# Performance work log

Hardware: AMD Instinct MI355X
Metric: run time of the kernel (lower is better)

## Reference

```python
import math
import jax, jax.numpy as jnp
import numpy as np

NUM_HEADS = 4
HEAD_DIM = 384


def reshape_fortran(x, shape):
    # column-major (Fortran) reshape, matching the torch reverse-permute trick
    x = jnp.transpose(x, tuple(reversed(range(x.ndim))))
    x = x.reshape(tuple(reversed(shape)))
    return jnp.transpose(x, tuple(reversed(range(len(shape)))))


def rel_pos_rotate(data):
    # data: [b, n_heads, L=2M-1, S] -> [b, n_heads, S, S]
    data = jnp.transpose(data, (0, 2, 3, 1))  # [b, d0=L, d1=S, d2=H]
    b, d0, d1, d2 = data.shape
    data = jnp.concatenate([data, jnp.zeros((b, d1, d1, d2), data.dtype)], axis=1)
    data = reshape_fortran(data, (b, (d0 + d1) * d1, 1, d2))
    data = data[:, :(d1 + d0 - 1) * d1]
    data = reshape_fortran(data, (b, d0 + d1 - 1, d1, d2))
    n = d0 // 2
    data = jnp.swapaxes(data[:, n:n + d1], 1, 2)  # [b, d1, d1, d2]
    return jnp.transpose(data, (0, 3, 1, 2))      # [b, H, S, S]


def setup_inputs() -> dict:
    key = jax.random.key(0)
    ks = jax.random.split(key, 5)
    B, S, D = 4, 920, 1536
    M = 920
    return {
        "hidden_states": jax.random.normal(ks[0], (B, S, D), jnp.float32),
        "q_w": jax.random.normal(ks[1], (D, NUM_HEADS * HEAD_DIM), jnp.float32) * 0.02,
        "k_w": jax.random.normal(ks[2], (D, NUM_HEADS * HEAD_DIM), jnp.float32) * 0.02,
        "v_w": jax.random.normal(ks[3], (D, NUM_HEADS * HEAD_DIM), jnp.float32) * 0.02,
        "dist_emb": jax.random.normal(ks[4], (2 * M - 1, HEAD_DIM), jnp.float32) * 0.02,
    }


def reference(hidden_states, q_w, k_w, v_w, dist_emb):
    B, S, D = hidden_states.shape

    def heads(x):  # [B,S,H*hd] -> [B,H,S,hd]
        return jnp.transpose(x.reshape(B, S, NUM_HEADS, HEAD_DIM), (0, 2, 1, 3))

    # query is pre-scaled by 1/sqrt(head_dim), matching the torch code
    q = heads((hidden_states @ q_w) / math.sqrt(HEAD_DIM))
    k = heads(hidden_states @ k_w)
    v = heads(hidden_states @ v_w)

    scores = jnp.einsum("bhqd,bhkd->bhqk", q, k)  # [B,H,S,S]
    # relative position scores: [B,H,L,S] then skew-rotated into [B,H,S,S]
    rel = jnp.einsum("ld,bhsd->bhls", dist_emb, q)
    scores = scores + rel_pos_rotate(rel)

    probs = jax.nn.softmax(scores, axis=-1)
    ctx = jnp.einsum("bhqk,bhkd->bhqd", probs, v)  # [B,H,S,hd]
    ctx = jnp.transpose(ctx, (0, 2, 1, 3)).reshape(B, S, NUM_HEADS * HEAD_DIM)
    return ctx
```

## Files before the change

kernel.cpp:

```cpp
#include <hip/hip_runtime.h>
#include <cstdint>
#include <cstddef>

#define SEQ   920
#define DM    1536
#define DH    384
#define NHD   4
#define NB    4
#define NBH   16
#define MTOK  3680
#define NREL  1839

typedef short          bf16x8 __attribute__((ext_vector_type(8)));
typedef float          f32x4  __attribute__((ext_vector_type(4)));
typedef unsigned short u16x4  __attribute__((ext_vector_type(4)));

__device__ __forceinline__ unsigned short f2bf(float f){
  union{float f; unsigned u;} v; v.f = f;
  unsigned r = v.u + 0x7FFFu + ((v.u >> 16) & 1u);
  return (unsigned short)(r >> 16);
}
__device__ __forceinline__ float bf2f(unsigned short h){
  union{unsigned u; float f;} v; v.u = ((unsigned)h) << 16;
  return v.f;
}
__device__ __forceinline__ f32x4 mfma_bf16(bf16x8 a, bf16x8 b, f32x4 c){
  return __builtin_amdgcn_mfma_f32_16x16x32_bf16(a, b, c, 0, 0, 0);
}
__device__ __forceinline__ void gload_lds16(const void* g, void* l){
  __builtin_amdgcn_global_load_lds((const __attribute__((address_space(1))) void*)g,
                                   (__attribute__((address_space(3))) void*)l, 16, 0, 0);
}

__global__ __launch_bounds__(256) void k_f2bf(const float* __restrict__ src,
                                              unsigned short* __restrict__ dst, int n){
  int i = (blockIdx.x * 256 + threadIdx.x) * 4;
  int stride = gridDim.x * 256 * 4;
  for(; i + 3 < n; i += stride){
    f32x4 v = *(const f32x4*)(src + i);
    u16x4 o; o.x = f2bf(v.x); o.y = f2bf(v.y); o.z = f2bf(v.z); o.w = f2bf(v.w);
    *(u16x4*)(dst + i) = o;
  }
}

__global__ __launch_bounds__(256) void k_wt(const float* __restrict__ w,
                                            unsigned short* __restrict__ wt, int which){
  __shared__ float t[32][33];
  int k0 = blockIdx.x * 32, n0 = blockIdx.y * 32;
  int tx = threadIdx.x, ty = threadIdx.y;
  #pragma unroll
  for(int j = 0; j < 4; j++)
    t[ty*4+j][tx] = w[(size_t)(k0 + ty*4 + j) * DM + n0 + tx];
  __syncthreads();
  #pragma unroll
  for(int j = 0; j < 4; j++)
    wt[(size_t)(which*DM + n0 + ty*4 + j) * DM + k0 + tx] = f2bf(t[tx][ty*4+j]);
}

template<class Epi>
__device__ __forceinline__ void gemm128(const unsigned short* A, int lda, int Amax,
                                        const unsigned short* B, int ldb, int Bmax,
                                        int K, int m0, int n0, Epi epi){
  __shared__ unsigned short As[128*32];
  __shared__ unsigned short Bs[128*32];
  const int tid = threadIdx.x, w = tid >> 6, l = tid & 63;
  const int lg = l >> 4, lo = l & 15;
  const int wm = (w >> 1) * 64, wn = (w & 1) * 64;
  f32x4 acc[4][4] = {};
  for(int k0 = 0; k0 < K; k0 += 32){
    __syncthreads();
    #pragma unroll
    for(int r = 0; r < 2; r++){
      int o = r*4096 + w*1024 + l*16;
      int row = o >> 6, c = o & 63;
      int ar = m0 + row; ar = ar < Amax ? ar : Amax - 1;
      gload_lds16((const char*)A + ((size_t)ar*lda + k0)*2 + c, (char*)As + o);
      int br = n0 + row; br = br < Bmax ? br : Bmax - 1;
      gload_lds16((const char*)B + ((size_t)br*ldb + k0)*2 + c, (char*)Bs + o);
    }
    __syncthreads();
    bf16x8 a[4], b[4];
    #pragma unroll
    for(int f = 0; f < 4; f++){
      a[f] = *(const bf16x8*)((const char*)As + (wm + f*16 + lo)*64 + lg*16);
      b[f] = *(const bf16x8*)((const char*)Bs + (wn + f*16 + lo)*64 + lg*16);
    }
    #pragma unroll
    for(int fi = 0; fi < 4; fi++)
      #pragma unroll
      for(int fj = 0; fj < 4; fj++)
        acc[fi][fj] = mfma_bf16(a[fi], b[fj], acc[fi][fj]);
  }
  #pragma unroll
  for(int fi = 0; fi < 4; fi++)
    #pragma unroll
    for(int fj = 0; fj < 4; fj++)
      #pragma unroll
      for(int i = 0; i < 4; i++){
        int m = m0 + wm + fi*16 + lg*4 + i;
        int n = n0 + wn + fj*16 + lo;
        epi(m, n, acc[fi][fj][i]);
      }
}

__global__ __launch_bounds__(256) void k_proj(const unsigned short* __restrict__ X,
                                              const unsigned short* __restrict__ Wt,
                                              unsigned short* __restrict__ Qb,
                                              unsigned short* __restrict__ Kb,
                                              unsigned short* __restrict__ Vt){
  int m0 = blockIdx.x * 128, n0 = blockIdx.y * 128;
  gemm128(X, DM, MTOK, Wt, DM, 3*DM, DM, m0, n0,
    [=] __device__ (int m, int n, float v){
      if(m >= MTOK) return;
      int b = m / SEQ, s = m % SEQ;
      int which = n / DM, r = n % DM, h = r / DH, d = r % DH;
      int bh = b * NHD + h;
      if(which == 0)      Qb[((size_t)bh*SEQ + s)*DH + d] = f2bf(v * 0.05103103630798287f);
      else if(which == 1) Kb[((size_t)bh*SEQ + s)*DH + d] = f2bf(v);
      else                Vt[((size_t)bh*DH + d)*SEQ + s] = f2bf(v);
    });
}

__global__ __launch_bounds__(256) void k_rel(const unsigned short* __restrict__ Qb,
                                             const unsigned short* __restrict__ E,
                                             unsigned short* __restrict__ relS){
  int m0 = blockIdx.x * 128, n0 = blockIdx.y * 128;
  gemm128(Qb, DH, NBH*SEQ, E, DH, NREL, DH, m0, n0,
    [=] __device__ (int m, int n, float v){
      int q = m % SEQ;
      int j = n - 919 + q;
      if(j < 0 || j >= SEQ) return;
      relS[(size_t)m*SEQ + j] = f2bf(v);
    });
}

__global__ __launch_bounds__(256) void k_attn(const unsigned short* __restrict__ Qb,
                                              const unsigned short* __restrict__ Kb,
                                              const unsigned short* __restrict__ Vt,
                                              const unsigned short* __restrict__ relS,
                                              float* __restrict__ out){
  __shared__ unsigned short Ks[32*384];
  __shared__ unsigned short Vs[384*32];
  __shared__ unsigned short Pl[32*40];
  __shared__ float sums[2][32];
  const int bh = blockIdx.y, qt = blockIdx.x, q0 = qt * 32;
  const int tid = threadIdx.x, w = tid >> 6, l = tid & 63;
  const int mi = w >> 1, ni = w & 1;
  const int lg = l >> 4, lo = l & 15;

  int qrow = q0 + mi*16 + lo; if(qrow > SEQ-1) qrow = SEQ-1;
  const char* Qrow = (const char*)(Qb + ((size_t)bh*SEQ + qrow)*DH);
  bf16x8 qf[12];
  #pragma unroll
  for(int ks = 0; ks < 12; ks++) qf[ks] = *(const bf16x8*)(Qrow + ks*64 + lg*16);

  f32x4 ctx[2][6] = {};
  float ps[4] = {0.f, 0.f, 0.f, 0.f};

  for(int kt = 0; kt < 29; kt++){
    const int k0 = kt * 32;
    __syncthreads();
    #pragma unroll
    for(int r = 0; r < 6; r++){
      int o = r*4096 + w*1024 + l*16;
      int row = o / 768, c = o - row*768;
      int csw = c ^ ((row & 7) << 4);
      int krow = k0 + row; if(krow > SEQ-1) krow = SEQ-1;
      gload_lds16((const char*)Kb + ((size_t)bh*SEQ + krow)*768 + csw, (char*)Ks + o);
      int d = o >> 6, c2 = o & 63;
      int vcol = k0*2 + c2; if(vcol > 1824) vcol = 1824;
      gload_lds16((const char*)Vt + ((size_t)bh*DH + d)*1840 + vcol, (char*)Vs + o);
    }
    __syncthreads();
    f32x4 accs = {};
    const int krowB = ni*16 + lo;
    const char* KsB = (const char*)Ks + krowB*768;
    const int sw = (krowB & 7) << 4;
    #pragma unroll
    for(int ks = 0; ks < 12; ks++){
      bf16x8 bf = *(const bf16x8*)(KsB + ((ks*64 + lg*16) ^ sw));
      accs = mfma_bf16(qf[ks], bf, accs);
    }
    unsigned short ph[4];
    #pragma unroll
    for(int i = 0; i < 4; i++){
      int q = q0 + mi*16 + lg*4 + i; if(q > SEQ-1) q = SEQ-1;
      int k = k0 + ni*16 + lo;
      int kc = k > SEQ-1 ? SEQ-1 : k;
      float rl = bf2f(relS[((size_t)bh*SEQ + q)*SEQ + kc]);
      float p = __expf(accs[i] + rl);
      if(k >= SEQ) p = 0.f;
      ps[i] += p;
      ph[i] = f2bf(p);
    }
    #pragma unroll
    for(int i = 0; i < 4; i++)
      *(unsigned short*)((char*)Pl + (mi*16 + lg*4 + i)*80 + (ni*16 + lo)*2) = ph[i];
    __syncthreads();
    bf16x8 pa0 = *(const bf16x8*)((char*)Pl + lo*80 + lg*16);
    bf16x8 pa1 = *(const bf16x8*)((char*)Pl + (16 + lo)*80 + lg*16);
    #pragma unroll
    for(int nj = 0; nj < 6; nj++){
      int d = w*96 + nj*16 + lo;
      bf16x8 vb = *(const bf16x8*)((char*)Vs + d*64 + lg*16);
      ctx[0][nj] = mfma_bf16(pa0, vb, ctx[0][nj]);
      ctx[1][nj] = mfma_bf16(pa1, vb, ctx[1][nj]);
    }
  }
  #pragma unroll
  for(int i = 0; i < 4; i++){
    float v = ps[i];
    v += __shfl_xor(v, 1); v += __shfl_xor(v, 2);
    v += __shfl_xor(v, 4); v += __shfl_xor(v, 8);
    if(lo == 0) sums[ni][mi*16 + lg*4 + i] = v;
  }
  __syncthreads();
  const int b = bh >> 2, h = bh & 3;
  #pragma unroll
  for(int m2 = 0; m2 < 2; m2++){
    #pragma unroll
    for(int i = 0; i < 4; i++){
      int ql = m2*16 + lg*4 + i;
      int q = q0 + ql;
      if(q >= SEQ) continue;
      float inv = 1.0f / (sums[0][ql] + sums[1][ql]);
      #pragma unroll
      for(int nj = 0; nj < 6; nj++){
        int d = w*96 + nj*16 + lo;
        out[((size_t)(b*SEQ + q))*DM + h*DH + d] = ctx[m2][nj][i] * inv;
      }
    }
  }
}

extern "C" void kernel_launch(void* const* d_in, const int* in_sizes, int n_in,
                              void* d_out, int out_size, void* d_ws, size_t ws_size,
                              hipStream_t stream){
  const float* X  = (const float*)d_in[0];
  const float* qw = (const float*)d_in[1];
  const float* kw = (const float*)d_in[2];
  const float* vw = (const float*)d_in[3];
  const float* de = (const float*)d_in[4];
  float* out = (float*)d_out;
  char* ws = (char*)d_ws;

  unsigned short* Qb   = (unsigned short*)ws;
  unsigned short* Kb   = (unsigned short*)(ws + 11304960);
  unsigned short* Vt   = (unsigned short*)(ws + 22609920);
  unsigned short* Eb   = (unsigned short*)(ws + 33914880);
  char* regionR        = ws + 35327232;
  unsigned short* relS = (unsigned short*)regionR;
  unsigned short* Xb   = (unsigned short*)regionR;
  unsigned short* Wt   = (unsigned short*)(regionR + 11304960);

  k_f2bf<<<dim3(1024), dim3(256), 0, stream>>>(X,  Xb, MTOK*DM);
  k_f2bf<<<dim3(256),  dim3(256), 0, stream>>>(de, Eb, NREL*DH);
  k_wt<<<dim3(48,48), dim3(32,8), 0, stream>>>(qw, Wt, 0);
  k_wt<<<dim3(48,48), dim3(32,8), 0, stream>>>(kw, Wt, 1);
  k_wt<<<dim3(48,48), dim3(32,8), 0, stream>>>(vw, Wt, 2);
  k_proj<<<dim3(29,36), dim3(256), 0, stream>>>(Xb, Wt, Qb, Kb, Vt);
  k_rel<<<dim3(115,15), dim3(256), 0, stream>>>(Qb, Eb, relS);
  k_attn<<<dim3(29,16), dim3(256), 0, stream>>>(Qb, Kb, Vt, relS, out);
}
```

Measured before the change: 243.2 us.

## Rewrite projection GEMMs with 192-tile triple-buffered pipeline and skip empty rel tiles

Replaces the 128x128 single-buffered GEMM with a 192x192 tile, 512-thread, three-stage async LDS pipeline using XOR-swizzled shared memory, explicit vmcnt waits and MFMA priority raising. The projection kernel gains a swizzled block-to-tile mapping for cache locality and vectorised V-transpose stores. The relative-position GEMM now exits early for tiles that fall entirely outside the skew band. The three weight-transpose launches are merged into one, and the conversion grids are enlarged. The larger LDS footprint (about 147 KB) and register usage lower occupancy, and the hand-written waitcnt counts depend on how many loads each stage issues.

New measurement: 212.3 us. 12.7% less time.

```diff
diff --git a/kernel.cpp b/kernel.cpp
--- a/kernel.cpp
+++ b/kernel.cpp
@@ -43,9 +43,12 @@
   }
 }
 
-__global__ __launch_bounds__(256) void k_wt(const float* __restrict__ w,
-                                            unsigned short* __restrict__ wt, int which){
+__global__ __launch_bounds__(256) void k_wt3(const float* __restrict__ qw,
+                                             const float* __restrict__ kw,
+                                             const float* __restrict__ vw,
+                                             unsigned short* __restrict__ wt){
   __shared__ float t[32][33];
+  const float* w = blockIdx.z == 0 ? qw : (blockIdx.z == 1 ? kw : vw);
   int k0 = blockIdx.x * 32, n0 = blockIdx.y * 32;
   int tx = threadIdx.x, ty = threadIdx.y;
   #pragma unroll
@@ -54,83 +57,152 @@
   __syncthreads();
   #pragma unroll
   for(int j = 0; j < 4; j++)
-    wt[(size_t)(which*DM + n0 + ty*4 + j) * DM + k0 + tx] = f2bf(t[tx][ty*4+j]);
+    wt[(size_t)(blockIdx.z*DM + n0 + ty*4 + j) * DM + k0 + tx] = f2bf(t[tx][ty*4+j]);
 }
 
 template<class Epi>
-__device__ __forceinline__ void gemm128(const unsigned short* A, int lda, int Amax,
-                                        const unsigned short* B, int ldb, int Bmax,
+__device__ __forceinline__ void gemm192(const unsigned short* __restrict__ A, int lda, int Amax,
+                                        const unsigned short* __restrict__ B, int ldb, int Bmax,
                                         int K, int m0, int n0, Epi epi){
-  __shared__ unsigned short As[128*32];
-  __shared__ unsigned short Bs[128*32];
-  const int tid = threadIdx.x, w = tid >> 6, l = tid & 63;
+  __shared__ unsigned short As[3*192*64];
+  __shared__ unsigned short Bs[3*192*64];
+  const int tid = threadIdx.x;
+  const int w = tid >> 6, l = tid & 63;
   const int lg = l >> 4, lo = l & 15;
-  const int wm = (w >> 1) * 64, wn = (w & 1) * 64;
-  f32x4 acc[4][4] = {};
-  for(int k0 = 0; k0 < K; k0 += 32){
-    __syncthreads();
-    #pragma unroll
-    for(int r = 0; r < 2; r++){
-      int o = r*4096 + w*1024 + l*16;
-      int row = o >> 6, c = o & 63;
-      int ar = m0 + row; ar = ar < Amax ? ar : Amax - 1;
-      gload_lds16((const char*)A + ((size_t)ar*lda + k0)*2 + c, (char*)As + o);
-      int br = n0 + row; br = br < Bmax ? br : Bmax - 1;
-      gload_lds16((const char*)B + ((size_t)br*ldb + k0)*2 + c, (char*)Bs + o);
-    }
-    __syncthreads();
-    bf16x8 a[4], b[4];
-    #pragma unroll
-    for(int f = 0; f < 4; f++){
-      a[f] = *(const bf16x8*)((const char*)As + (wm + f*16 + lo)*64 + lg*16);
-      b[f] = *(const bf16x8*)((const char*)Bs + (wn + f*16 + lo)*64 + lg*16);
-    }
-    #pragma unroll
-    for(int fi = 0; fi < 4; fi++)
-      #pragma unroll
-      for(int fj = 0; fj < 4; fj++)
-        acc[fi][fj] = mfma_bf16(a[fi], b[fj], acc[fi][fj]);
-  }
-  #pragma unroll
-  for(int fi = 0; fi < 4; fi++)
-    #pragma unroll
-    for(int fj = 0; fj < 4; fj++)
-      #pragma unroll
-      for(int i = 0; i < 4; i++){
-        int m = m0 + wm + fi*16 + lg*4 + i;
-        int n = n0 + wn + fj*16 + lo;
-        epi(m, n, acc[fi][fj][i]);
-      }
-}
-
-__global__ __launch_bounds__(256) void k_proj(const unsigned short* __restrict__ X,
+  const int wm = w >> 2, wn = w & 3;
+
+  const char* ga[3]; const char* gb[3];
+  #pragma unroll
+  for(int r = 0; r < 3; r++){
+    int row = r*64 + (tid >> 3);
+    int gslot = (tid & 7) ^ (row & 7);
+    int ar = m0 + row; ar = ar < Amax ? ar : Amax - 1;
+    ga[r] = (const char*)A + (size_t)ar*lda*2 + gslot*16;
+    int br = n0 + row; br = br < Bmax ? br : Bmax - 1;
+    gb[r] = (const char*)B + (size_t)br*ldb*2 + gslot*16;
+  }
+  const int ldst = tid * 16;
+
+  auto stage = [&](int kt, int slot){
+    size_t koff = (size_t)kt * 128;
+    #pragma unroll
+    for(int r = 0; r < 3; r++){
+      gload_lds16(ga[r] + koff, (char*)As + slot*24576 + r*8192 + ldst);
+      gload_lds16(gb[r] + koff, (char*)Bs + slot*24576 + r*8192 + ldst);
+    }
+  };
+
+  f32x4 acc[6][3] = {};
+  const int sw = (lo & 7) << 4;
+
+  auto compute = [&](int slot){
+    const char* Ab = (const char*)As + slot*24576;
+    const char* Bb = (const char*)Bs + slot*24576;
+    bf16x8 af[6][2], bf[3][2];
+    #pragma unroll
+    for(int fi = 0; fi < 6; fi++){
+      int row = wm*96 + fi*16 + lo;
+      #pragma unroll
+      for(int kk = 0; kk < 2; kk++)
+        af[fi][kk] = *(const bf16x8*)(Ab + row*128 + ((kk*64 + lg*16) ^ sw));
+    }
+    #pragma unroll
+    for(int fj = 0; fj < 3; fj++){
+      int row = wn*48 + fj*16 + lo;
+      #pragma unroll
+      for(int kk = 0; kk < 2; kk++)
+        bf[fj][kk] = *(const bf16x8*)(Bb + row*128 + ((kk*64 + lg*16) ^ sw));
+    }
+    __builtin_amdgcn_s_setprio(1);
+    #pragma unroll
+    for(int kk = 0; kk < 2; kk++)
+      #pragma unroll
+      for(int fi = 0; fi < 6; fi++)
+        #pragma unroll
+        for(int fj = 0; fj < 3; fj++)
+          acc[fi][fj] = mfma_bf16(af[fi][kk], bf[fj][kk], acc[fi][fj]);
+    __builtin_amdgcn_s_setprio(0);
+  };
+
+  const int nk = K >> 6;
+  stage(0, 0);
+  stage(1, 1);
+  int st = 0;
+  for(int t = 0; t < nk; t++){
+    if(t + 2 < nk){
+      int s2 = st + 2 >= 3 ? st - 1 : st + 2;
+      stage(t + 2, s2);
+      asm volatile("s_waitcnt vmcnt(12)" ::: "memory");
+    } else if(t + 1 < nk){
+      asm volatile("s_waitcnt vmcnt(6)" ::: "memory");
+    } else {
+      asm volatile("s_waitcnt vmcnt(0)" ::: "memory");
+    }
+    __builtin_amdgcn_s_barrier();
+    compute(st);
+    __builtin_amdgcn_s_barrier();
+    st = st + 1 >= 3 ? 0 : st + 1;
+  }
+
+  #pragma unroll
+  for(int fi = 0; fi < 6; fi++)
+    #pragma unroll
+    for(int fj = 0; fj < 3; fj++){
+      int m = m0 + wm*96 + fi*16 + lg*4;
+      int n = n0 + wn*48 + fj*16 + lo;
+      epi(m, n, acc[fi][fj]);
+    }
+}
+
+__global__ __launch_bounds__(512) void k_proj(const unsigned short* __restrict__ X,
                                               const unsigned short* __restrict__ Wt,
                                               unsigned short* __restrict__ Qb,
                                               unsigned short* __restrict__ Kb,
                                               unsigned short* __restrict__ Vt){
-  int m0 = blockIdx.x * 128, n0 = blockIdx.y * 128;
-  gemm128(X, DM, MTOK, Wt, DM, 3*DM, DM, m0, n0,
-    [=] __device__ (int m, int n, float v){
+  int bid = blockIdx.x;
+  int wg  = (bid & 7) * 60 + (bid >> 3);
+  int m0 = (wg % 20) * 192, n0 = (wg / 20) * 192;
+  gemm192(X, DM, MTOK, Wt, DM, 3*DM, DM, m0, n0,
+    [=] __device__ (int m, int n, f32x4 v4){
       if(m >= MTOK) return;
+      int which = n / DM, r = n % DM, h = r / DH, d = r % DH;
       int b = m / SEQ, s = m % SEQ;
-      int which = n / DM, r = n % DM, h = r / DH, d = r % DH;
       int bh = b * NHD + h;
-      if(which == 0)      Qb[((size_t)bh*SEQ + s)*DH + d] = f2bf(v * 0.05103103630798287f);
-      else if(which == 1) Kb[((size_t)bh*SEQ + s)*DH + d] = f2bf(v);
-      else                Vt[((size_t)bh*DH + d)*SEQ + s] = f2bf(v);
+      if(which == 2){
+        u16x4 o;
+        o.x = f2bf(v4.x); o.y = f2bf(v4.y); o.z = f2bf(v4.z); o.w = f2bf(v4.w);
+        *(u16x4*)(Vt + ((size_t)bh*DH + d)*SEQ + s) = o;
+      } else if(which == 0){
+        #pragma unroll
+        for(int i = 0; i < 4; i++)
+          Qb[((size_t)bh*SEQ + s + i)*DH + d] = f2bf(v4[i] * 0.05103103630798287f);
+      } else {
+        #pragma unroll
+        for(int i = 0; i < 4; i++)
+          Kb[((size_t)bh*SEQ + s + i)*DH + d] = f2bf(v4[i]);
+      }
     });
 }
 
-__global__ __launch_bounds__(256) void k_rel(const unsigned short* __restrict__ Qb,
+__global__ __launch_bounds__(512) void k_rel(const unsigned short* __restrict__ Qb,
                                              const unsigned short* __restrict__ E,
                                              unsigned short* __restrict__ relS){
-  int m0 = blockIdx.x * 128, n0 = blockIdx.y * 128;
-  gemm128(Qb, DH, NBH*SEQ, E, DH, NREL, DH, m0, n0,
-    [=] __device__ (int m, int n, float v){
-      int q = m % SEQ;
-      int j = n - 919 + q;
-      if(j < 0 || j >= SEQ) return;
-      relS[(size_t)m*SEQ + j] = f2bf(v);
+  int m0 = blockIdx.x * 192, n0 = blockIdx.y * 192;
+  int s0 = m0 % SEQ;
+  int qlo = s0, qhi = s0 + 191;
+  if(qhi >= SEQ){ qlo = 0; qhi = SEQ - 1; }
+  if(n0 + 191 < 919 - qhi || n0 > 1838 - qlo) return;
+  gemm192(Qb, DH, NBH*SEQ, E, DH, NREL, DH, m0, n0,
+    [=] __device__ (int m, int n, f32x4 v4){
+      #pragma unroll
+      for(int i = 0; i < 4; i++){
+        int mi = m + i;
+        if(mi >= NBH*SEQ) continue;
+        int q = mi % SEQ;
+        int j = n - 919 + q;
+        if(j < 0 || j >= SEQ) continue;
+        relS[(size_t)mi*SEQ + j] = f2bf(v4[i]);
+      }
     });
 }
 
@@ -253,12 +325,10 @@
   unsigned short* Xb   = (unsigned short*)regionR;
   unsigned short* Wt   = (unsigned short*)(regionR + 11304960);
 
-  k_f2bf<<<dim3(1024), dim3(256), 0, stream>>>(X,  Xb, MTOK*DM);
-  k_f2bf<<<dim3(256),  dim3(256), 0, stream>>>(de, Eb, NREL*DH);
-  k_wt<<<dim3(48,48), dim3(32,8), 0, stream>>>(qw, Wt, 0);
-  k_wt<<<dim3(48,48), dim3(32,8), 0, stream>>>(kw, Wt, 1);
-  k_wt<<<dim3(48,48), dim3(32,8), 0, stream>>>(vw, Wt, 2);
-  k_proj<<<dim3(29,36), dim3(256), 0, stream>>>(Xb, Wt, Qb, Kb, Vt);
-  k_rel<<<dim3(115,15), dim3(256), 0, stream>>>(Qb, Eb, relS);
+  k_f2bf<<<dim3(2048), dim3(256), 0, stream>>>(X,  Xb, MTOK*DM);
+  k_f2bf<<<dim3(690),  dim3(256), 0, stream>>>(de, Eb, NREL*DH);
+  k_wt3<<<dim3(48,48,3), dim3(32,8), 0, stream>>>(qw, kw, vw, Wt);
+  k_proj<<<dim3(480), dim3(512), 0, stream>>>(Xb, Wt, Qb, Kb, Vt);
+  k_rel<<<dim3(77,10), dim3(512), 0, stream>>>(Qb, Eb, relS);
   k_attn<<<dim3(29,16), dim3(256), 0, stream>>>(Qb, Kb, Vt, relS, out);
 }
```
